# Kernel tuning notes

Hardware: AMD Instinct MI355X
Metric: run time of the kernel (lower is better)

Reference implementation:

```python
import jax, jax.numpy as jnp
import numpy as np

K = 32            # spatial kernel: neighbors per anchor
STRIDE = 4        # spatial_stride -> S = N // 4 anchors
TK_HALF = 1       # temporal_kernel_size=3 -> window offsets -1,0,+1


def setup_inputs() -> dict:
    key = jax.random.key(0)
    k1, k2, k3 = jax.random.split(key, 3)
    points = jax.random.normal(k1, (2, 4, 8192, 6), dtype=jnp.float32)
    # conv_d: Conv2d(4 -> 64, 1x1, bias=False) as a dense matrix [out,in]
    Wd = jax.random.normal(k2, (64, 4), dtype=jnp.float32) * 0.1
    # mlp: Conv2d(64 -> 128, 1x1, bias=False)
    Wm = jax.random.normal(k3, (128, 64), dtype=jnp.float32) * 0.1
    return {"points": points, "Wd": Wd, "Wm": Wm}


def _fps(xyz, npoint):
    """Farthest point sampling on a single frame. xyz: [N,3] -> idx [npoint] int32.
    Deterministic start at index 0."""
    d0 = jnp.sum((xyz - xyz[0]) ** 2, axis=-1)  # [N]

    def body(dists, _):
        nxt = jnp.argmax(dists)
        d = jnp.sum((xyz - xyz[nxt]) ** 2, axis=-1)
        return jnp.minimum(dists, d), nxt.astype(jnp.int32)

    _, idxs = jax.lax.scan(body, d0, None, length=npoint - 1)
    return jnp.concatenate([jnp.zeros((1,), jnp.int32), idxs])


def _knn_idx(neighbor_xyz, anchor_xyz, k):
    """Adaptive ball query realized as k-nearest-neighbors.
    neighbor_xyz: [B,N,3], anchor_xyz: [B,S,3] -> idx [B,S,k]."""
    d2 = jnp.sum((anchor_xyz[:, :, None, :] - neighbor_xyz[:, None, :, :]) ** 2, axis=-1)  # [B,S,N]
    _, idx = jax.lax.top_k(-d2, k)
    return idx


def _group(pts, idx):
    """pts: [B,N,C], idx: [B,S,K] -> [B,S,K,C] gather per batch."""
    return jax.vmap(lambda p, i: p[i])(pts, idx)


def reference(points, Wd, Wm):
    xyzs = points[..., :3]                       # [B,L,N,3] (rgb unused when in_planes==0)
    B, L, N, _ = xyzs.shape
    S = N // STRIDE
    # replicate temporal padding [1,1]
    pad = jnp.concatenate([xyzs[:, :1], xyzs, xyzs[:, -1:]], axis=1)  # [B,L+2,N,3]

    new_xyzs, new_feats = [], []
    for t in range(TK_HALF, L + 2 - TK_HALF):    # anchor frames in padded indexing
        frame = pad[:, t]                        # [B,N,3]
        aidx = jax.vmap(lambda x: _fps(x, S))(frame)       # [B,S]
        anchor = _group(frame, aidx[:, :, None])[:, :, 0]  # [B,S,3]

        fsum = jnp.zeros((B, S, Wm.shape[0]), dtype=points.dtype)
        for di in range(-TK_HALF, TK_HALF + 1):
            nb = pad[:, t + di]                              # [B,N,3]
            idx = _knn_idx(nb, anchor, K)                    # [B,S,K]
            grouped = _group(nb, idx)                        # [B,S,K,3]
            disp = grouped - anchor[:, :, None, :]           # xyz displacement
            tdisp = jnp.full((B, S, K, 1), float(di), dtype=points.dtype)
            d4 = jnp.concatenate([disp, tdisp], axis=-1)     # [B,S,K,4]
            h = jax.nn.relu(jnp.einsum('bskc,oc->bsko', d4, Wd))   # conv_d + ReLU
            h = jax.nn.relu(jnp.einsum('bsko,po->bskp', h, Wm))    # mlp + ReLU
            fsum = fsum + jnp.max(h, axis=2)                 # spatial max-pool, temporal sum
        new_xyzs.append(anchor)
        new_feats.append(fsum)

    new_xyzs = jnp.stack(new_xyzs, axis=1)                   # [B,T,S,3]
    new_feats = jnp.stack(new_feats, axis=1).transpose(0, 1, 3, 2)  # [B,T,C,S]
    return new_xyzs, new_feats
```

## Files before the change

### kernel.cpp

```cpp
#include <hip/hip_runtime.h>
#include <stdint.h>

#define NPTS 8192
#define NS   2048
#define KNNK 32

typedef unsigned long long u64;
typedef float f32x2 __attribute__((ext_vector_type(2)));

__global__ __launch_bounds__(512)
void fps_kernel(const float* __restrict__ pts,
                float* __restrict__ out_xyz)
{
#pragma clang fp contract(off)
    const int bt  = blockIdx.x;
    const int tid = threadIdx.x;
    const float* frame = pts + (size_t)bt * NPTS * 6;

    __shared__ float4 p4[NPTS];
    __shared__ u64 ring[3];

    f32x2 x2[8], y2[8], z2[8], dd2[8];
#pragma unroll
    for (int j = 0; j < 16; ++j) {
        int n = j * 512 + tid;
        float x = frame[n*6+0], y = frame[n*6+1], z = frame[n*6+2];
        x2[j >> 1][j & 1] = x;
        y2[j >> 1][j & 1] = y;
        z2[j >> 1][j & 1] = z;
        dd2[j >> 1][j & 1] = 3.4028234663852886e38f;
        p4[n] = make_float4(x, y, z, 0.0f);
    }
    if (tid < 3) ring[tid] = 0;
    if (tid == 0) {
        float* ow = out_xyz + (size_t)bt * NS * 3;
        ow[0] = x2[0][0]; ow[1] = y2[0][0]; ow[2] = z2[0][0];
    }
    __syncthreads();
    float sx = p4[0].x, sy = p4[0].y, sz = p4[0].z;

    int r = 1;
    for (int i = 1; i < NS; ++i) {
        f32x2 sxv = {sx, sx}, syv = {sy, sy}, szv = {sz, sz};
        f32x2 m2 = {0.0f, 0.0f};
#pragma unroll
        for (int q = 0; q < 8; ++q) {
            f32x2 dx = x2[q] - sxv;
            f32x2 dy = y2[q] - syv;
            f32x2 dz = z2[q] - szv;
            f32x2 dd = (dx*dx + dy*dy) + dz*dz;
            f32x2 nd;
            nd[0] = fminf(dd2[q][0], dd[0]);
            nd[1] = fminf(dd2[q][1], dd[1]);
            dd2[q] = nd;
            m2[0] = fmaxf(m2[0], nd[0]);
            m2[1] = fmaxf(m2[1], nd[1]);
        }
        float mloc = fmaxf(m2[0], m2[1]);
        int bestn = 0;
#pragma unroll
        for (int j = 15; j >= 0; --j)
            bestn = (dd2[j >> 1][j & 1] == mloc) ? (j * 512 + tid) : bestn;
        u64 key = ((u64)__float_as_uint(mloc) << 32) | (unsigned)(8191 - bestn);
#pragma unroll
        for (int off = 32; off > 0; off >>= 1) {
            u64 o = __shfl_xor(key, off, 64);
            key = (o > key) ? o : key;
        }
        if ((tid & 63) == 0) atomicMax(&ring[r], key);
        int rn = r + 1; if (rn == 3) rn = 0;
        if (tid == 0) ring[rn] = 0;
        __syncthreads();
        u64 k = ring[r];
        int idx = 8191 - (int)(k & 0xFFFFFFFFu);
        float4 c = p4[idx];
        sx = c.x; sy = c.y; sz = c.z;
        if (tid == 0) {
            float* ow = out_xyz + ((size_t)bt * NS + i) * 3;
            ow[0] = sx; ow[1] = sy; ow[2] = sz;
        }
        r = rn;
    }
}

__device__ __forceinline__ void knn_compact(u64* st, int lane, int& cnt, float& rk_f)
{
    for (int e = 0; e < 32; ++e)
        if (e >= cnt) st[(e + 32) * 64 + lane] = ~0ull;
    for (int k = 2; k <= 32; k <<= 1)
        for (int j = k >> 1; j > 0; j >>= 1)
            for (int i = 0; i < 32; ++i) {
                int l = i ^ j;
                if (l > i) {
                    u64 a = st[(i + 32) * 64 + lane];
                    u64 b = st[(l + 32) * 64 + lane];
                    bool asc = ((i & k) == 0);
                    if ((a > b) == asc) {
                        st[(i + 32) * 64 + lane] = b;
                        st[(l + 32) * 64 + lane] = a;
                    }
                }
            }
    for (int i = 0; i < 32; ++i) {
        u64 a = st[i * 64 + lane];
        u64 b = st[(63 - i) * 64 + lane];
        if (b < a) st[i * 64 + lane] = b;
    }
    for (int j = 16; j > 0; j >>= 1)
        for (int i = 0; i < 32; ++i) {
            int l = i ^ j;
            if (l > i) {
                u64 a = st[i * 64 + lane];
                u64 b = st[l * 64 + lane];
                if (a > b) {
                    st[i * 64 + lane] = b;
                    st[l * 64 + lane] = a;
                }
            }
        }
    rk_f = __uint_as_float((unsigned)(st[31 * 64 + lane] >> 32));
    cnt = 0;
}

__global__ __launch_bounds__(128)
void knn_kernel(const float* __restrict__ pts,
                const float* __restrict__ anchors,
                unsigned short* __restrict__ knn_out)
{
    const int blk  = blockIdx.x;
    const int bt   = blk / 96;
    const int rr   = blk % 96;
    const int di   = rr / 32;
    const int sblk = rr % 32;
    const int b = bt >> 2, t0 = bt & 3;
    int lnb = t0 + di - 1; lnb = lnb < 0 ? 0 : (lnb > 3 ? 3 : lnb);
    const float* nb = pts + (size_t)(b * 4 + lnb) * NPTS * 6;
    const int tid  = threadIdx.x;
    const int w    = tid >> 6;
    const int lane = tid & 63;
    const int s    = sblk * 64 + lane;

    const float* ap = anchors + ((size_t)bt * NS + s) * 3;
    float ax = ap[0], ay = ap[1], az = ap[2];

    __shared__ u64 st[2][64 * 64];
    __shared__ u64 trash[64];
    __shared__ float4 tile[2][256];
    u64* stw = st[w];

    for (int e = 0; e < 64; ++e) stw[e * 64 + lane] = ~0ull;
    float rk_f = __uint_as_float(0xFFFFFFFFu);
    int cnt = 0;

    const int cbase = w * 4096;
    for (int tb = 0; tb < 16; ++tb) {
        __syncthreads();
#pragma unroll
        for (int q = 0; q < 4; ++q) {
            int c = q * 64 + lane;
            int n = cbase + tb * 256 + c;
            tile[w][c] = make_float4(nb[n*6+0], nb[n*6+1], nb[n*6+2], 0.0f);
        }
        __syncthreads();
        for (int c0 = 0; c0 < 256; c0 += 8) {
#pragma unroll
            for (int j = 0; j < 8; ++j) {
                float4 qv = tile[w][c0 + j];
                float dx = __fsub_rn(ax, qv.x);
                float dy = __fsub_rn(ay, qv.y);
                float dz = __fsub_rn(az, qv.z);
                float d2 = __fadd_rn(__fadd_rn(__fmul_rn(dx,dx), __fmul_rn(dy,dy)),
                                     __fmul_rn(dz,dz));
                u64 key = ((u64)__float_as_uint(d2) << 32)
                        | (unsigned)(cbase + tb * 256 + c0 + j);
                bool p = !(d2 > rk_f);
                u64* dst = p ? &stw[(32 + cnt) * 64 + lane] : &trash[lane];
                *dst = key;
                cnt += p ? 1 : 0;
            }
            if (__any(cnt >= 24)) knn_compact(stw, lane, cnt, rk_f);
        }
    }
    knn_compact(stw, lane, cnt, rk_f);
    __syncthreads();

    if (w == 0) {
        unsigned short* op = knn_out + (((size_t)bt * 3 + di) * NS + s) * KNNK;
#pragma unroll
        for (int e = 0; e < 32; ++e) {
            u64 a = st[0][e * 64 + lane];
            u64 c = st[1][(31 - e) * 64 + lane];
            u64 m = c < a ? c : a;
            op[e] = (unsigned short)(m & 0xFFFFull);
        }
    }
}

__global__ __launch_bounds__(256)
void mlp_kernel(const float* __restrict__ pts,
                const float* __restrict__ anchors,
                const unsigned short* __restrict__ knn,
                const float* __restrict__ Wd,
                const float* __restrict__ Wm,
                float* __restrict__ out_feats)
{
    const int blk = blockIdx.x;
    const int bt  = blk >> 9;
    const int sq  = blk & 511;
    const int b = bt >> 2, t0 = bt & 3;
    const int tid = threadIdx.x;
    const int a   = tid >> 6;
    const int r   = tid & 63;
    const int p0  = (r & 15) * 8;
    const int kt  = r >> 4;
    const int k0  = kt * 8;
    const int s   = sq * 4 + a;

    __shared__ float WmT[64 * 128];
    __shared__ float Wds[256];
    __shared__ float h1[4][64][32];
    __shared__ float d4s[4][32][4];
    __shared__ float pmax[4][4][128];

    for (int i = tid; i < 8192; i += 256) {
        int pp = i >> 6, oo = i & 63;
        WmT[oo * 128 + pp] = Wm[i];
    }
    Wds[tid] = Wd[tid];

    float fsum0 = 0.0f, fsum1 = 0.0f;

    for (int dd = 0; dd < 3; ++dd) {
        __syncthreads();
        if (tid < 128) {
            int sa = tid >> 5, k = tid & 31;
            int ss = sq * 4 + sa;
            int lnb = t0 + dd - 1; lnb = lnb < 0 ? 0 : (lnb > 3 ? 3 : lnb);
            const float* nbf = pts + (size_t)(b*4 + lnb) * NPTS * 6;
            const float* ap = anchors + ((size_t)bt * NS + ss) * 3;
            int idx = knn[(((size_t)bt*3 + dd) * NS + ss) * KNNK + k];
            d4s[sa][k][0] = nbf[idx*6+0] - ap[0];
            d4s[sa][k][1] = nbf[idx*6+1] - ap[1];
            d4s[sa][k][2] = nbf[idx*6+2] - ap[2];
            d4s[sa][k][3] = (float)(dd - 1);
        }
        __syncthreads();
        {
            int k  = r & 31;
            int oh = r >> 5;
            float4 dv = *(const float4*)&d4s[a][k][0];
#pragma unroll
            for (int ii = 0; ii < 32; ++ii) {
                int o = oh * 32 + ii;
                float4 wv = *(const float4*)&Wds[o * 4];
                float h = fmaf(dv.x, wv.x, fmaf(dv.y, wv.y,
                             fmaf(dv.z, wv.z, dv.w * wv.w)));
                h1[a][o][k] = fmaxf(h, 0.0f);
            }
        }
        __syncthreads();
        float acc[8][8];
#pragma unroll
        for (int i = 0; i < 8; ++i)
#pragma unroll
            for (int j = 0; j < 8; ++j) acc[i][j] = 0.0f;
        for (int o = 0; o < 64; ++o) {
            float4 wv0 = *(const float4*)&WmT[o * 128 + p0];
            float4 wv1 = *(const float4*)&WmT[o * 128 + p0 + 4];
            float4 h0 = *(const float4*)&h1[a][o][k0];
            float4 h4 = *(const float4*)&h1[a][o][k0 + 4];
            float hw[8] = {h0.x, h0.y, h0.z, h0.w, h4.x, h4.y, h4.z, h4.w};
#pragma unroll
            for (int i = 0; i < 8; ++i) {
                float ww = (i < 4) ? ((i == 0) ? wv0.x : (i == 1) ? wv0.y :
                                      (i == 2) ? wv0.z : wv0.w)
                                   : ((i == 4) ? wv1.x : (i == 5) ? wv1.y :
                                      (i == 6) ? wv1.z : wv1.w);
#pragma unroll
                for (int j = 0; j < 8; ++j)
                    acc[i][j] = fmaf(ww, hw[j], acc[i][j]);
            }
        }
        float4 pmA, pmB;
#pragma unroll
        for (int i = 0; i < 8; ++i) {
            float m = acc[i][0];
#pragma unroll
            for (int j = 1; j < 8; ++j) m = fmaxf(m, acc[i][j]);
            if (i < 4) ((float*)&pmA)[i] = m;
            else       ((float*)&pmB)[i - 4] = m;
        }
        *(float4*)&pmax[a][kt][p0]     = pmA;
        *(float4*)&pmax[a][kt][p0 + 4] = pmB;
        __syncthreads();
        float m0 = fmaxf(fmaxf(pmax[a][0][r], pmax[a][1][r]),
                         fmaxf(pmax[a][2][r], pmax[a][3][r]));
        float m1 = fmaxf(fmaxf(pmax[a][0][r + 64], pmax[a][1][r + 64]),
                         fmaxf(pmax[a][2][r + 64], pmax[a][3][r + 64]));
        fsum0 += fmaxf(m0, 0.0f);
        fsum1 += fmaxf(m1, 0.0f);
    }
    out_feats[((size_t)bt * 128 + r) * NS + s]        = fsum0;
    out_feats[((size_t)bt * 128 + r + 64) * NS + s]   = fsum1;
}

extern "C" void kernel_launch(void* const* d_in, const int* in_sizes, int n_in,
                              void* d_out, int out_size, void* d_ws, size_t ws_size,
                              hipStream_t stream)
{
    const float* pts = (const float*)d_in[0];
    const float* Wd  = (const float*)d_in[1];
    const float* Wm  = (const float*)d_in[2];

    float* out_xyz   = (float*)d_out;
    float* out_feats = out_xyz + 8 * NS * 3;

    unsigned short* knn = (unsigned short*)d_ws;

    fps_kernel<<<8, 512, 0, stream>>>(pts, out_xyz);
    knn_kernel<<<8 * 3 * 32, 128, 0, stream>>>(pts, out_xyz, knn);
    mlp_kernel<<<8 * (NS / 4), 256, 0, stream>>>(pts, out_xyz, knn, Wd, Wm, out_feats);
}
```

Measured before the change: 3.603 ms.

## Keep KNN top-32 list and bitonic merge in registers instead of LDS

```diff
diff --git a/kernel.cpp b/kernel.cpp
--- a/kernel.cpp
+++ b/kernel.cpp
@@ -83,42 +83,47 @@
     }
 }
 
-__device__ __forceinline__ void knn_compact(u64* st, int lane, int& cnt, float& rk_f)
-{
-    for (int e = 0; e < 32; ++e)
-        if (e >= cnt) st[(e + 32) * 64 + lane] = ~0ull;
-    for (int k = 2; k <= 32; k <<= 1)
-        for (int j = k >> 1; j > 0; j >>= 1)
+__device__ __forceinline__ void knn_compact_reg(u64 (&mn)[32], const u64* bufLDS,
+                                                int lane, int& cnt, float& rk_f)
+{
+    u64 b[32];
+#pragma unroll
+    for (int e = 0; e < 32; ++e) {
+        u64 v = bufLDS[e * 64 + lane];
+        b[e] = (e < cnt) ? v : ~0ull;
+    }
+#pragma unroll
+    for (int k = 2; k <= 32; k <<= 1) {
+#pragma unroll
+        for (int j = k >> 1; j > 0; j >>= 1) {
+#pragma unroll
             for (int i = 0; i < 32; ++i) {
                 int l = i ^ j;
                 if (l > i) {
-                    u64 a = st[(i + 32) * 64 + lane];
-                    u64 b = st[(l + 32) * 64 + lane];
                     bool asc = ((i & k) == 0);
-                    if ((a > b) == asc) {
-                        st[(i + 32) * 64 + lane] = b;
-                        st[(l + 32) * 64 + lane] = a;
-                    }
+                    u64 x = b[i], y = b[l];
+                    if ((x > y) == asc) { b[i] = y; b[l] = x; }
                 }
             }
+        }
+    }
+#pragma unroll
     for (int i = 0; i < 32; ++i) {
-        u64 a = st[i * 64 + lane];
-        u64 b = st[(63 - i) * 64 + lane];
-        if (b < a) st[i * 64 + lane] = b;
-    }
-    for (int j = 16; j > 0; j >>= 1)
+        u64 y = b[31 - i];
+        if (y < mn[i]) mn[i] = y;
+    }
+#pragma unroll
+    for (int j = 16; j > 0; j >>= 1) {
+#pragma unroll
         for (int i = 0; i < 32; ++i) {
             int l = i ^ j;
             if (l > i) {
-                u64 a = st[i * 64 + lane];
-                u64 b = st[l * 64 + lane];
-                if (a > b) {
-                    st[i * 64 + lane] = b;
-                    st[l * 64 + lane] = a;
-                }
-            }
-        }
-    rk_f = __uint_as_float((unsigned)(st[31 * 64 + lane] >> 32));
+                u64 x = mn[i], y = mn[l];
+                if (x > y) { mn[i] = y; mn[l] = x; }
+            }
+        }
+    }
+    rk_f = __uint_as_float((unsigned)(mn[31] >> 32));
     cnt = 0;
 }
 
@@ -143,12 +148,14 @@
     const float* ap = anchors + ((size_t)bt * NS + s) * 3;
     float ax = ap[0], ay = ap[1], az = ap[2];
 
-    __shared__ u64 st[2][64 * 64];
-    __shared__ u64 trash[64];
-    __shared__ float4 tile[2][256];
-    u64* stw = st[w];
-
-    for (int e = 0; e < 64; ++e) stw[e * 64 + lane] = ~0ull;
+    __shared__ __align__(16) float tx[2][256];
+    __shared__ __align__(16) float ty[2][256];
+    __shared__ __align__(16) float tz[2][256];
+    __shared__ u64 buf[2][33][64];
+
+    u64 mn[32];
+#pragma unroll
+    for (int e = 0; e < 32; ++e) mn[e] = ~0ull;
     float rk_f = __uint_as_float(0xFFFFFFFFu);
     int cnt = 0;
 
@@ -159,38 +166,49 @@
         for (int q = 0; q < 4; ++q) {
             int c = q * 64 + lane;
             int n = cbase + tb * 256 + c;
-            tile[w][c] = make_float4(nb[n*6+0], nb[n*6+1], nb[n*6+2], 0.0f);
-        }
-        __syncthreads();
-        for (int c0 = 0; c0 < 256; c0 += 8) {
-#pragma unroll
-            for (int j = 0; j < 8; ++j) {
-                float4 qv = tile[w][c0 + j];
-                float dx = __fsub_rn(ax, qv.x);
-                float dy = __fsub_rn(ay, qv.y);
-                float dz = __fsub_rn(az, qv.z);
+            tx[w][c] = nb[n*6+0];
+            ty[w][c] = nb[n*6+1];
+            tz[w][c] = nb[n*6+2];
+        }
+        __syncthreads();
+        for (int g = 0; g < 64; ++g) {
+            float4 xs = ((const float4*)&tx[w][0])[g];
+            float4 ys = ((const float4*)&ty[w][0])[g];
+            float4 zs = ((const float4*)&tz[w][0])[g];
+            int n0 = cbase + tb * 256 + g * 4;
+#pragma unroll
+            for (int jj = 0; jj < 4; ++jj) {
+                float qx = jj==0?xs.x:jj==1?xs.y:jj==2?xs.z:xs.w;
+                float qy = jj==0?ys.x:jj==1?ys.y:jj==2?ys.z:ys.w;
+                float qz = jj==0?zs.x:jj==1?zs.y:jj==2?zs.z:zs.w;
+                float dx = __fsub_rn(ax, qx);
+                float dy = __fsub_rn(ay, qy);
+                float dz = __fsub_rn(az, qz);
                 float d2 = __fadd_rn(__fadd_rn(__fmul_rn(dx,dx), __fmul_rn(dy,dy)),
                                      __fmul_rn(dz,dz));
-                u64 key = ((u64)__float_as_uint(d2) << 32)
-                        | (unsigned)(cbase + tb * 256 + c0 + j);
                 bool p = !(d2 > rk_f);
-                u64* dst = p ? &stw[(32 + cnt) * 64 + lane] : &trash[lane];
-                *dst = key;
+                int row = p ? cnt : 32;
+                buf[w][row][lane] = ((u64)__float_as_uint(d2) << 32)
+                                  | (unsigned)(n0 + jj);
                 cnt += p ? 1 : 0;
             }
-            if (__any(cnt >= 24)) knn_compact(stw, lane, cnt, rk_f);
-        }
-    }
-    knn_compact(stw, lane, cnt, rk_f);
+            if (__any(cnt >= 28))
+                knn_compact_reg(mn, &buf[w][0][0], lane, cnt, rk_f);
+        }
+    }
+    knn_compact_reg(mn, &buf[w][0][0], lane, cnt, rk_f);
     __syncthreads();
-
+    if (w == 1) {
+#pragma unroll
+        for (int e = 0; e < 32; ++e) buf[1][e][lane] = mn[e];
+    }
+    __syncthreads();
     if (w == 0) {
         unsigned short* op = knn_out + (((size_t)bt * 3 + di) * NS + s) * KNNK;
 #pragma unroll
         for (int e = 0; e < 32; ++e) {
-            u64 a = st[0][e * 64 + lane];
-            u64 c = st[1][(31 - e) * 64 + lane];
-            u64 m = c < a ? c : a;
+            u64 c = buf[1][31 - e][lane];
+            u64 m = c < mn[e] ? c : mn[e];
             op[e] = (unsigned short)(m & 0xFFFFull);
         }
     }
```

Measured after the change: 2.974 ms. -17.5%, faster.
